# Optimization experiments

Hardware: AMD Instinct MI355X
Metric: run time of the kernel (lower is better)

The kernel has to match this reference:

```python
import jax, jax.numpy as jnp
import numpy as np

N = 100000      # nodes
E = 1600000     # edges
IN = 256        # in_channels
H = 128         # hidden_channels
OUT = 64        # output_channels
B = 64          # graphs in batch
EPS = 1e-5      # BatchNorm eps


def setup_inputs() -> dict:
    key = jax.random.key(0)
    ks = jax.random.split(key, 32)

    def lin_w(k, fan_in, fan_out):
        return (jax.random.normal(k, (fan_in, fan_out), jnp.float32) / np.sqrt(fan_in)).astype(jnp.float32)

    inp = {
        'x': jax.random.normal(ks[0], (N, IN), jnp.float32),
        'edge_index': jax.random.randint(ks[1], (2, E), 0, N, dtype=jnp.int32),
        'batch': jnp.sort(jax.random.randint(ks[2], (N,), 0, B, dtype=jnp.int32)),
        # GCN conv weights (layer 0: IN->H, layers 1,2: H->H)
        'W0': lin_w(ks[3], IN, H), 'b0': jnp.zeros((H,), jnp.float32),
        'W1': lin_w(ks[4], H, H),  'b1': jnp.zeros((H,), jnp.float32),
        'W2': lin_w(ks[5], H, H),  'b2': jnp.zeros((H,), jnp.float32),
        # BatchNorm affine params per layer
        'g0': 1.0 + 0.1 * jax.random.normal(ks[6], (H,), jnp.float32),
        'be0': 0.1 * jax.random.normal(ks[7], (H,), jnp.float32),
        'g1': 1.0 + 0.1 * jax.random.normal(ks[8], (H,), jnp.float32),
        'be1': 0.1 * jax.random.normal(ks[9], (H,), jnp.float32),
        'g2': 1.0 + 0.1 * jax.random.normal(ks[10], (H,), jnp.float32),
        'be2': 0.1 * jax.random.normal(ks[11], (H,), jnp.float32),
        # residual projection (in_channels != hidden_channels)
        'Wres': lin_w(ks[12], IN, H), 'bres': jnp.zeros((H,), jnp.float32),
        # head MLP: Linear(H,H) -> ReLU -> Dropout(eval) -> Linear(H,OUT)
        'Wl0': lin_w(ks[13], H, H), 'bl0': jnp.zeros((H,), jnp.float32),
        'Wl1': lin_w(ks[14], H, OUT), 'bl1': jnp.zeros((OUT,), jnp.float32),
    }
    return inp


def _gcn_layer(h, src, dst, dinv, W, b):
    # PyG GCNConv: linear first, then sym-normalized aggregation with self loops
    h = h @ W                                   # [N, d_out]
    enorm = dinv[src] * dinv[dst]               # [E]
    msg = h[src] * enorm[:, None]               # gather + scale  [E, d_out]
    agg = jax.ops.segment_sum(msg, dst, num_segments=N)
    agg = agg + h * (dinv * dinv)[:, None]      # self-loop contribution (norm = 1/deg)
    return agg + b


def _bn_eval(h, g, be):
    # inference BatchNorm with running_mean=0, running_var=1
    return h * (g / np.sqrt(1.0 + EPS)) + be


def reference(x, edge_index, batch,
              W0, b0, W1, b1, W2, b2,
              g0, be0, g1, be1, g2, be2,
              Wres, bres, Wl0, bl0, Wl1, bl1):
    src, dst = edge_index[0], edge_index[1]
    # degrees with self loops (edge weight 1)
    deg = jax.ops.segment_sum(jnp.ones((E,), jnp.float32), dst, num_segments=N) + 1.0
    dinv = jax.lax.rsqrt(deg)                   # [N]

    Ws, bs, gs, bes = [W0, W1, W2], [b0, b1, b2], [g0, g1, g2], [be0, be1, be2]
    h = x
    for i in range(3):
        h = _gcn_layer(h, src, dst, dinv, Ws[i], bs[i])
        h = jax.nn.relu(_bn_eval(h, gs[i], bes[i]))  # dropout is identity in eval
        if i == 0:
            h = h + (x @ Wres + bres)           # residual projection of original input

    # head MLP on node features
    out = jax.nn.relu(h @ Wl0 + bl0) @ Wl1 + bl1    # [N, OUT]

    # global mean pool over graphs
    counts = jax.ops.segment_sum(jnp.ones((N,), jnp.float32), batch, num_segments=B)
    pooled = jax.ops.segment_sum(h, batch, num_segments=B) / jnp.maximum(counts, 1.0)[:, None]
    return out, pooled
```

## Files before the change

kernel.cpp:

```cpp
#include <hip/hip_runtime.h>
#include <hip/hip_fp16.h>

typedef __half f16;
typedef _Float16 half8 __attribute__((ext_vector_type(8)));
typedef float floatx4 __attribute__((ext_vector_type(4)));

#define NN   100000
#define NE   1600000
#define CIN  256
#define CH   128
#define COUT 64
#define NB   64

#define NBUK 128
#define NPB  782
#define BCAP 32
#define CAPB 20480
#define G1   512
#define EPB  3125
#define CSZ  15104

__global__ void k_sentinel(float* __restrict__ out, int n, float val) {
    int i = blockIdx.x * 256 + threadIdx.x;
    if (i < n) out[i] = val;
}

__global__ void k_init(float* __restrict__ pool, float* __restrict__ cnt,
                       int* __restrict__ gcur) {
    int i = blockIdx.x * 256 + threadIdx.x;
    if (i < NB * CH) pool[i] = 0.0f;
    if (i < NB) cnt[i] = 0.0f;
    if (i < NBUK) gcur[i] = i * CAPB;
}

__global__ __launch_bounds__(256) void k_bin(const int* __restrict__ src,
                                             const int* __restrict__ dst,
                                             int* __restrict__ gcur,
                                             int* __restrict__ stage) {
    __shared__ int bins[NBUK][BCAP];
    __shared__ int bcnt[NBUK];
    __shared__ int fcnt[NBUK];
    __shared__ int fbase[NBUK];
    const int tid = threadIdx.x;
    if (tid < NBUK) bcnt[tid] = 0;
    __syncthreads();
    const int e0 = blockIdx.x * EPB;
    const int e1 = (e0 + EPB < NE) ? e0 + EPB : NE;
    for (int base = e0; base < e1; base += 256) {
        int e = base + tid;
        if (e < e1) {
            int s = src[e], d = dst[e];
            int bk = d / NPB;
            int pk = ((d - bk * NPB) << 17) | s;
            int pos = atomicAdd(&bcnt[bk], 1);
            if (pos < BCAP) {
                bins[bk][pos] = pk;
            } else {
                int gp = atomicAdd(&gcur[bk], 1);
                if (gp < (bk + 1) * CAPB) stage[gp] = pk;
            }
        }
        __syncthreads();
        if (tid < NBUK) {
            int stored = bcnt[tid]; if (stored > BCAP) stored = BCAP;
            int nf = stored & ~15;
            fcnt[tid] = nf;
            if (nf) fbase[tid] = atomicAdd(&gcur[tid], nf);
        }
        __syncthreads();
#pragma unroll
        for (int pass = 0; pass < NBUK / 16; ++pass) {
            int b = pass * 16 + (tid >> 4);
            int sl = tid & 15;
            int nf = fcnt[b];
            int fb = fbase[b];
            for (int k = sl; k < nf; k += 16)
                if (fb + k < (b + 1) * CAPB) stage[fb + k] = bins[b][k];
        }
        __syncthreads();
        if (tid < NBUK) {
            int stored = bcnt[tid]; if (stored > BCAP) stored = BCAP;
            int nf = fcnt[tid];
            for (int k = nf; k < stored; ++k) bins[tid][k - nf] = bins[tid][k];
            bcnt[tid] = stored - nf;
        }
        __syncthreads();
    }
    if (tid < NBUK) {
        int stored = bcnt[tid];
        fcnt[tid] = stored;
        if (stored) fbase[tid] = atomicAdd(&gcur[tid], stored);
    }
    __syncthreads();
#pragma unroll
    for (int pass = 0; pass < NBUK / 16; ++pass) {
        int b = pass * 16 + (tid >> 4);
        int sl = tid & 15;
        int nf = fcnt[b];
        int fb = fbase[b];
        for (int k = sl; k < nf; k += 16)
            if (fb + k < (b + 1) * CAPB) stage[fb + k] = bins[b][k];
    }
}

__global__ void k_gtot(const int* __restrict__ gcur, int* __restrict__ barr,
                       int* __restrict__ rowptr) {
    int lane = threadIdx.x;
    int carry = 0;
    for (int c0 = 0; c0 < NBUK; c0 += 64) {
        int idx = c0 + lane;
        int orig = gcur[idx] - idx * CAPB;
        int v = orig;
#pragma unroll
        for (int off = 1; off < 64; off <<= 1) {
            int t = __shfl_up(v, off);
            if (lane >= off) v += t;
        }
        barr[idx] = v - orig + carry;
        carry += __shfl(v, 63);
    }
    if (lane == 0) rowptr[NN] = NE;
}

__global__ __launch_bounds__(256) void k_csr(const int* __restrict__ gcur,
                                             const int* __restrict__ barr,
                                             const int* __restrict__ stage,
                                             int* __restrict__ rowptr,
                                             int* __restrict__ csr,
                                             float* __restrict__ dinv) {
    __shared__ int hist[NPB];
    __shared__ int lcsr[CSZ];
    const int b = blockIdx.x, tid = threadIdx.x;
    const int nbase = b * NPB;
    const int nloc = (NPB < NN - nbase) ? NPB : NN - nbase;
    const int count = gcur[b] - b * CAPB;
    const int gbase = barr[b];
    const int sb = b * CAPB;
    for (int i = tid; i < NPB; i += 256) hist[i] = 0;
    __syncthreads();
    for (int i = tid; i < count; i += 256)
        atomicAdd(&hist[stage[sb + i] >> 17], 1);
    __syncthreads();
    for (int dl = tid; dl < nloc; dl += 256)
        dinv[nbase + dl] = rsqrtf((float)hist[dl] + 1.0f);
    __syncthreads();
    if (tid < 64) {
        int carry = 0;
        for (int c0 = 0; c0 < NPB; c0 += 64) {
            int idx = c0 + tid;
            int orig = (idx < NPB) ? hist[idx] : 0;
            int v = orig;
#pragma unroll
            for (int off = 1; off < 64; off <<= 1) {
                int t = __shfl_up(v, off);
                if (tid >= off) v += t;
            }
            if (idx < NPB) hist[idx] = v - orig + carry;
            carry += __shfl(v, 63);
        }
    }
    __syncthreads();
    for (int dl = tid; dl < nloc; dl += 256)
        rowptr[nbase + dl] = gbase + hist[dl];
    __syncthreads();
    const bool fits = (count <= CSZ);
    for (int i = tid; i < count; i += 256) {
        int pk = stage[sb + i];
        int dl = pk >> 17, s = pk & 0x1FFFF;
        int pos = atomicAdd(&hist[dl], 1);
        if (fits) lcsr[pos] = s;
        else csr[gbase + pos] = s;
    }
    __syncthreads();
    if (fits)
        for (int i = tid; i < count; i += 256) csr[gbase + i] = lcsr[i];
}

__global__ __launch_bounds__(256) void k_wconv(
        const float* __restrict__ W0, const float* __restrict__ Wres,
        const float* __restrict__ W1, const float* __restrict__ W2,
        const float* __restrict__ Wl0, const float* __restrict__ Wl1,
        half8* __restrict__ F0, half8* __restrict__ Fres,
        half8* __restrict__ F1, half8* __restrict__ F2,
        half8* __restrict__ Fl0, half8* __restrict__ Fl1) {
    int f = blockIdx.x * 256 + threadIdx.x;
    const float* W; half8* F; int M, base;
    if      (f <  4096) { W = W0;   F = F0;   M = 128; base = 0; }
    else if (f <  8192) { W = Wres; F = Fres; M = 128; base = 4096; }
    else if (f < 10240) { W = W1;   F = F1;   M = 128; base = 8192; }
    else if (f < 12288) { W = W2;   F = F2;   M = 128; base = 10240; }
    else if (f < 14336) { W = Wl0;  F = Fl0;  M = 128; base = 12288; }
    else if (f < 15360) { W = Wl1;  F = Fl1;  M = 64;  base = 14336; }
    else return;
    int fl = f - base;
    int lane = fl & 63, fm = lane & 15, g = lane >> 4;
    int rest = fl >> 6;
    int nt = M / 16;
    int t = rest % nt, kt = rest / nt;
    half8 v;
#pragma unroll
    for (int j = 0; j < 8; ++j)
        v[j] = (_Float16)W[(size_t)(kt * 32 + g * 8 + j) * M + t * 16 + fm];
    F[fl] = v;
}

__global__ __launch_bounds__(256) void k_mfma0(const float* __restrict__ x,
                                               const half8* __restrict__ WF,
                                               const half8* __restrict__ WFb,
                                               const float* __restrict__ bres,
                                               const float* __restrict__ dinv,
                                               f16* __restrict__ lout,
                                               f16* __restrict__ rout) {
    constexpr int LP = 72;
    __shared__ __align__(16) _Float16 Al[2][64 * LP];
    const int tid = threadIdx.x;
    const int wave = tid >> 6, lane = tid & 63;
    const int fm = lane & 15, g = lane >> 4;
    const int rb = blockIdx.x * 64;

    const int arow = tid >> 2;
    const int koff = (tid & 3) * 16;
    const int grow = rb + arow;
    const bool live = (grow < NN);
    const float* xp = x + (size_t)(live ? grow : 0) * CIN + koff;

    floatx4 acc[16];
#pragma unroll
    for (int t = 0; t < 16; ++t)
#pragma unroll
        for (int r = 0; r < 4; ++r) acc[t][r] = 0.0f;

    auto ldchunk = [&](int kbase, half8& h0, half8& h1) {
        if (live) {
            float4 a = *(const float4*)(xp + kbase);
            float4 b = *(const float4*)(xp + kbase + 4);
            float4 c = *(const float4*)(xp + kbase + 8);
            float4 d = *(const float4*)(xp + kbase + 12);
            h0[0] = (_Float16)a.x; h0[1] = (_Float16)a.y;
            h0[2] = (_Float16)a.z; h0[3] = (_Float16)a.w;
            h0[4] = (_Float16)b.x; h0[5] = (_Float16)b.y;
            h0[6] = (_Float16)b.z; h0[7] = (_Float16)b.w;
            h1[0] = (_Float16)c.x; h1[1] = (_Float16)c.y;
            h1[2] = (_Float16)c.z; h1[3] = (_Float16)c.w;
            h1[4] = (_Float16)d.x; h1[5] = (_Float16)d.y;
            h1[6] = (_Float16)d.z; h1[7] = (_Float16)d.w;
        } else {
#pragma unroll
            for (int i = 0; i < 8; ++i) { h0[i] = (_Float16)0.0f; h1[i] = (_Float16)0.0f; }
        }
    };

    {
        half8 h0, h1;
        ldchunk(0, h0, h1);
        *(half8*)&Al[0][arow * LP + koff] = h0;
        *(half8*)&Al[0][arow * LP + koff + 8] = h1;
    }
    __syncthreads();

    for (int kt = 0; kt < 4; ++kt) {
        const int cur = kt & 1;
        half8 n0, n1;
        if (kt < 3) ldchunk((kt + 1) * 64, n0, n1);
#pragma unroll
        for (int s = 0; s < 2; ++s) {
            half8 afrag = *(const half8*)&Al[cur][(wave * 16 + fm) * LP + s * 32 + g * 8];
            const int kk = kt * 2 + s;
#pragma unroll
            for (int t = 0; t < 8; ++t)
                acc[t] = __builtin_amdgcn_mfma_f32_16x16x32_f16(
                    afrag, WF[((size_t)kk * 8 + t) * 64 + lane], acc[t], 0, 0, 0);
#pragma unroll
            for (int t = 0; t < 8; ++t)
                acc[8 + t] = __builtin_amdgcn_mfma_f32_16x16x32_f16(
                    afrag, WFb[((size_t)kk * 8 + t) * 64 + lane], acc[8 + t], 0, 0, 0);
        }
        if (kt < 3) {
            *(half8*)&Al[cur ^ 1][arow * LP + koff] = n0;
            *(half8*)&Al[cur ^ 1][arow * LP + koff + 8] = n1;
        }
        __syncthreads();
    }

    const int rloc = wave * 16 + g * 4;
#pragma unroll
    for (int t = 0; t < 8; ++t) {
        int col = t * 16 + fm;
#pragma unroll
        for (int r = 0; r < 4; ++r) {
            int row = rb + rloc + r;
            if (row < NN) lout[(size_t)row * 128 + col] = (f16)(acc[t][r] * dinv[row]);
        }
    }
#pragma unroll
    for (int t = 0; t < 8; ++t) {
        int col = t * 16 + fm;
        float bb = bres[col];
#pragma unroll
        for (int r = 0; r < 4; ++r) {
            int row = rb + rloc + r;
            if (row < NN) rout[(size_t)row * 128 + col] = (f16)(acc[8 + t][r] + bb);
        }
    }
}

__global__ __launch_bounds__(256) void k_lin(const f16* __restrict__ A,
                                             const half8* __restrict__ WF,
                                             const float* __restrict__ dinv,
                                             f16* __restrict__ lout) {
    const int tid = threadIdx.x;
    const int wave = tid >> 6, lane = tid & 63;
    const int fm = lane & 15, g = lane >> 4;
    const int tb = blockIdx.x * 64 + wave * 16;
    const int arow = tb + fm;

    half8 af[4];
#pragma unroll
    for (int kt = 0; kt < 4; ++kt) {
        if (arow < NN) {
            af[kt] = *(const half8*)((const _Float16*)A + (size_t)arow * CH + kt * 32 + g * 8);
        } else {
#pragma unroll
            for (int i = 0; i < 8; ++i) af[kt][i] = (_Float16)0.0f;
        }
    }

    floatx4 acc[8];
#pragma unroll
    for (int t = 0; t < 8; ++t)
#pragma unroll
        for (int r = 0; r < 4; ++r) acc[t][r] = 0.0f;

#pragma unroll
    for (int kt = 0; kt < 4; ++kt)
#pragma unroll
        for (int t = 0; t < 8; ++t)
            acc[t] = __builtin_amdgcn_mfma_f32_16x16x32_f16(
                af[kt], WF[((size_t)kt * 8 + t) * 64 + lane], acc[t], 0, 0, 0);

#pragma unroll
    for (int t = 0; t < 8; ++t) {
        int col = t * 16 + fm;
#pragma unroll
        for (int r = 0; r < 4; ++r) {
            int row = tb + g * 4 + r;
            if (row < NN) lout[(size_t)row * CH + col] = (f16)(acc[t][r] * dinv[row]);
        }
    }
}

__global__ __launch_bounds__(256) void k_head(const f16* __restrict__ A,
                                              const half8* __restrict__ WF0,
                                              const half8* __restrict__ WF1,
                                              const float* __restrict__ bl0,
                                              const float* __restrict__ bl1,
                                              float* __restrict__ outp) {
    constexpr int LP = 136;
    __shared__ __align__(16) _Float16 Hs[64 * LP];
    const int tid = threadIdx.x;
    const int wave = tid >> 6, lane = tid & 63;
    const int fm = lane & 15, g = lane >> 4;
    const int tb = blockIdx.x * 64 + wave * 16;
    const int arow = tb + fm;

    half8 af[4];
#pragma unroll
    for (int kt = 0; kt < 4; ++kt) {
        if (arow < NN) {
            af[kt] = *(const half8*)((const _Float16*)A + (size_t)arow * CH + kt * 32 + g * 8);
        } else {
#pragma unroll
            for (int i = 0; i < 8; ++i) af[kt][i] = (_Float16)0.0f;
        }
    }

    floatx4 acc[8];
#pragma unroll
    for (int t = 0; t < 8; ++t)
#pragma unroll
        for (int r = 0; r < 4; ++r) acc[t][r] = 0.0f;

#pragma unroll
    for (int kt = 0; kt < 4; ++kt)
#pragma unroll
        for (int t = 0; t < 8; ++t)
            acc[t] = __builtin_amdgcn_mfma_f32_16x16x32_f16(
                af[kt], WF0[((size_t)kt * 8 + t) * 64 + lane], acc[t], 0, 0, 0);

    const int lrow = wave * 16 + g * 4;
#pragma unroll
    for (int t = 0; t < 8; ++t) {
        int col = t * 16 + fm;
        float b = bl0[col];
#pragma unroll
        for (int r = 0; r < 4; ++r)
            Hs[(lrow + r) * LP + col] = (_Float16)fmaxf(acc[t][r] + b, 0.0f);
    }
    __syncthreads();

    floatx4 acc2[4];
#pragma unroll
    for (int t = 0; t < 4; ++t)
#pragma unroll
        for (int r = 0; r < 4; ++r) acc2[t][r] = 0.0f;

#pragma unroll
    for (int kt = 0; kt < 4; ++kt) {
        half8 a2 = *(const half8*)&Hs[(wave * 16 + fm) * LP + kt * 32 + g * 8];
#pragma unroll
        for (int t = 0; t < 4; ++t)
            acc2[t] = __builtin_amdgcn_mfma_f32_16x16x32_f16(
                a2, WF1[((size_t)kt * 4 + t) * 64 + lane], acc2[t], 0, 0, 0);
    }

#pragma unroll
    for (int t = 0; t < 4; ++t) {
        int col = t * 16 + fm;
        float b = bl1[col];
#pragma unroll
        for (int r = 0; r < 4; ++r) {
            int row = tb + g * 4 + r;
            if (row < NN) outp[(size_t)row * COUT + col] = acc2[t][r] + b;
        }
    }
}

template <bool RES>
__global__ __launch_bounds__(256) void k_gather(const int* __restrict__ rowptr,
                                                const int* __restrict__ csr,
                                                const float* __restrict__ dinv,
                                                const f16* __restrict__ lin,
                                                const f16* __restrict__ res,
                                                f16* __restrict__ h,
                                                const float* __restrict__ b,
                                                const float* __restrict__ g,
                                                const float* __restrict__ be) {
    const int gw = (blockIdx.x * 256 + threadIdx.x) >> 6;
    const int lane = threadIdx.x & 63;
    if (gw >= NN) return;
    const __half2* lp = (const __half2*)lin;
    const int start = __builtin_amdgcn_readfirstlane(rowptr[gw]);
    const int end   = __builtin_amdgcn_readfirstlane(rowptr[gw + 1]);

    float2 acc = __half22float2(lp[(size_t)gw * 64 + lane]);
    int j = start;
    for (; j + 7 < end; j += 8) {
        int s0 = csr[j],     s1 = csr[j + 1], s2 = csr[j + 2], s3 = csr[j + 3];
        int s4 = csr[j + 4], s5 = csr[j + 5], s6 = csr[j + 6], s7 = csr[j + 7];
        float2 v0 = __half22float2(lp[(size_t)s0 * 64 + lane]);
        float2 v1 = __half22float2(lp[(size_t)s1 * 64 + lane]);
        float2 v2 = __half22float2(lp[(size_t)s2 * 64 + lane]);
        float2 v3 = __half22float2(lp[(size_t)s3 * 64 + lane]);
        float2 v4 = __half22float2(lp[(size_t)s4 * 64 + lane]);
        float2 v5 = __half22float2(lp[(size_t)s5 * 64 + lane]);
        float2 v6 = __half22float2(lp[(size_t)s6 * 64 + lane]);
        float2 v7 = __half22float2(lp[(size_t)s7 * 64 + lane]);
        acc.x += ((v0.x + v1.x) + (v2.x + v3.x)) + ((v4.x + v5.x) + (v6.x + v7.x));
        acc.y += ((v0.y + v1.y) + (v2.y + v3.y)) + ((v4.y + v5.y) + (v6.y + v7.y));
    }
    for (; j + 3 < end; j += 4) {
        int s0 = csr[j], s1 = csr[j + 1], s2 = csr[j + 2], s3 = csr[j + 3];
        float2 v0 = __half22float2(lp[(size_t)s0 * 64 + lane]);
        float2 v1 = __half22float2(lp[(size_t)s1 * 64 + lane]);
        float2 v2 = __half22float2(lp[(size_t)s2 * 64 + lane]);
        float2 v3 = __half22float2(lp[(size_t)s3 * 64 + lane]);
        acc.x += (v0.x + v1.x) + (v2.x + v3.x);
        acc.y += (v0.y + v1.y) + (v2.y + v3.y);
    }
    for (; j < end; ++j) {
        int s = csr[j];
        float2 v = __half22float2(lp[(size_t)s * 64 + lane]);
        acc.x += v.x;
        acc.y += v.y;
    }
    const float inv_sqrt = 0.99999500003749968f;
    float dv = dinv[gw];
    int f = lane * 2;
    float2 bb = *(const float2*)&b[f];
    float2 gg = *(const float2*)&g[f];
    float2 ee = *(const float2*)&be[f];
    float t0 = fmaxf((acc.x * dv + bb.x) * (gg.x * inv_sqrt) + ee.x, 0.0f);
    float t1 = fmaxf((acc.y * dv + bb.y) * (gg.y * inv_sqrt) + ee.y, 0.0f);
    if (RES) {
        float2 rv = __half22float2(((const __half2*)res)[(size_t)gw * 64 + lane]);
        t0 += rv.x;
        t1 += rv.y;
    }
    ((__half2*)h)[(size_t)gw * 64 + lane] = __floats2half2_rn(t0, t1);
}

__global__ void k_count(const int* __restrict__ batch, float* __restrict__ cnt) {
    __shared__ float hist[NB];
    int tid = threadIdx.x;
    if (tid < NB) hist[tid] = 0.0f;
    __syncthreads();
    int n = blockIdx.x * 256 + tid;
    if (n < NN) atomicAdd(&hist[batch[n]], 1.0f);
    __syncthreads();
    if (tid < NB && hist[tid] != 0.0f) atomicAdd(&cnt[tid], hist[tid]);
}

__global__ void k_pool(const f16* __restrict__ h, const int* __restrict__ batch,
                       float* __restrict__ pool) {
    int n0 = blockIdx.x * 64;
    int j = threadIdx.x;
    int cur = batch[n0];
    float acc = 0.0f;
    int nend = (n0 + 64 < NN) ? n0 + 64 : NN;
    for (int n = n0; n < nend; ++n) {
        int b = batch[n];
        if (b != cur) {
            atomicAdd(&pool[cur * CH + j], acc);
            acc = 0.0f;
            cur = b;
        }
        acc += (float)h[(size_t)n * CH + j];
    }
    atomicAdd(&pool[cur * CH + j], acc);
}

__global__ void k_pool_fin(const float* __restrict__ pool,
                           const float* __restrict__ cnt,
                           float* __restrict__ out) {
    int i = blockIdx.x * 256 + threadIdx.x;
    if (i < NB * CH) {
        float c = fmaxf(cnt[i / CH], 1.0f);
        out[i] = pool[i] / c;
    }
}

extern "C" void kernel_launch(void* const* d_in, const int* in_sizes, int n_in,
                              void* d_out, int out_size, void* d_ws, size_t ws_size,
                              hipStream_t stream) {
    float* outp  = (float*)d_out;
    float* poolp = outp + (size_t)NN * COUT;

    const size_t HB = (size_t)NN * CH * 2;
    const size_t LB = (size_t)NN * CH * 2;
    const size_t RB = (size_t)NN * CH * 2;
    const size_t DV = (size_t)NN * 4;
    const size_t RP = 400016;
    const size_t CS = (size_t)NE * 4;
    const size_t GC = 512;
    const size_t BA = 528;
    const size_t PL = (size_t)NB * CH * 4;
    const size_t CT = 256;
    const size_t F0B = 4096 * 16, F1B = 2048 * 16, FLB = 1024 * 16;
    const size_t need = HB + LB + RB + DV + RP + CS + GC + BA + PL + CT
                        + 2 * F0B + 3 * F1B + FLB;
    if (ws_size < need) {
        k_sentinel<<<(out_size + 255) / 256, 256, 0, stream>>>(outp, out_size, 2000.0f);
        return;
    }
    char* p = (char*)d_ws;
    f16*   hbuf   = (f16*)p;               p += HB;
    f16*   lbuf   = (f16*)p;               p += LB;
    f16*   rbuf   = (f16*)p;
    int*   stage  = (int*)p;               p += RB;
    float* dinv   = (float*)p;             p += DV;
    int*   rowptr = (int*)p;               p += RP;
    int*   csr    = (int*)p;               p += CS;
    int*   gcur   = (int*)p;               p += GC;
    int*   barr   = (int*)p;               p += BA;
    float* pool   = (float*)p;             p += PL;
    float* cnt    = (float*)p;             p += CT;
    half8* F0     = (half8*)p;             p += F0B;
    half8* Fres   = (half8*)p;             p += F0B;
    half8* F1     = (half8*)p;             p += F1B;
    half8* F2     = (half8*)p;             p += F1B;
    half8* Fl0    = (half8*)p;             p += F1B;
    half8* Fl1    = (half8*)p;

    const float* x   = (const float*)d_in[0];
    const int*   ei  = (const int*)d_in[1];
    const int*   bat = (const int*)d_in[2];
    const float* W0 = (const float*)d_in[3],  *b0 = (const float*)d_in[4];
    const float* W1 = (const float*)d_in[5],  *b1 = (const float*)d_in[6];
    const float* W2 = (const float*)d_in[7],  *b2 = (const float*)d_in[8];
    const float* g0 = (const float*)d_in[9],  *be0 = (const float*)d_in[10];
    const float* g1 = (const float*)d_in[11], *be1 = (const float*)d_in[12];
    const float* g2 = (const float*)d_in[13], *be2 = (const float*)d_in[14];
    const float* Wres = (const float*)d_in[15], *bres = (const float*)d_in[16];
    const float* Wl0 = (const float*)d_in[17], *bl0 = (const float*)d_in[18];
    const float* Wl1 = (const float*)d_in[19], *bl1 = (const float*)d_in[20];

    const int* src = ei;
    const int* dst = ei + NE;

    const int gRow = (NN + 63) / 64;
    const int gGat = (NN * 64) / 256;

    k_init<<<33, 256, 0, stream>>>(pool, cnt, gcur);
    k_wconv<<<60, 256, 0, stream>>>(W0, Wres, W1, W2, Wl0, Wl1,
                                    F0, Fres, F1, F2, Fl0, Fl1);
    k_bin<<<G1, 256, 0, stream>>>(src, dst, gcur, stage);
    k_gtot<<<1, 64, 0, stream>>>(gcur, barr, rowptr);
    k_csr<<<NBUK, 256, 0, stream>>>(gcur, barr, stage, rowptr, csr, dinv);

    k_mfma0<<<gRow, 256, 0, stream>>>(x, F0, Fres, bres, dinv, lbuf, rbuf);
    k_gather<true><<<gGat, 256, 0, stream>>>(rowptr, csr, dinv, lbuf, rbuf, hbuf, b0, g0, be0);

    k_lin<<<gRow, 256, 0, stream>>>(hbuf, F1, dinv, lbuf);
    k_gather<false><<<gGat, 256, 0, stream>>>(rowptr, csr, dinv, lbuf, nullptr, hbuf, b1, g1, be1);

    k_lin<<<gRow, 256, 0, stream>>>(hbuf, F2, dinv, lbuf);
    k_gather<false><<<gGat, 256, 0, stream>>>(rowptr, csr, dinv, lbuf, nullptr, hbuf, b2, g2, be2);

    k_count<<<(NN + 255) / 256, 256, 0, stream>>>(bat, cnt);
    k_pool<<<gRow, 128, 0, stream>>>(hbuf, bat, pool);
    k_pool_fin<<<(NB * CH + 255) / 256, 256, 0, stream>>>(pool, cnt, poolp);

    k_head<<<gRow, 256, 0, stream>>>(hbuf, Fl0, Fl1, bl0, bl1, outp);
}
```

Before: 694.1 us.

## Stage weight fragments in shared memory for layer-0 MFMA GEMM

Changes the first-layer GEMM (x@W0 and x@Wres) so each wave loads a quarter of the B fragments from global into registers and stores them to a double-buffered LDS tile, instead of every wave reading all B fragments from global directly. The K tile is halved from 64 to 32 and the loop runs 8 iterations, which shrinks the A tile and its padding. The intent is to cut redundant global and L2 traffic for weights and to overlap weight loads with MFMA work. In exchange it adds more LDS traffic and twice as many barriers.

```diff
diff --git a/kernel.cpp b/kernel.cpp
--- a/kernel.cpp
+++ b/kernel.cpp
@@ -211,74 +211,81 @@
                                                const float* __restrict__ dinv,
                                                f16* __restrict__ lout,
                                                f16* __restrict__ rout) {
-    constexpr int LP = 72;
-    __shared__ __align__(16) _Float16 Al[2][64 * LP];
+    constexpr int APAD = 40;
+    __shared__ __align__(16) _Float16 Al[2][64 * APAD];
+    __shared__ __align__(16) _Float16 Bl[2][16 * 512];
     const int tid = threadIdx.x;
     const int wave = tid >> 6, lane = tid & 63;
     const int fm = lane & 15, g = lane >> 4;
     const int rb = blockIdx.x * 64;
 
     const int arow = tid >> 2;
-    const int koff = (tid & 3) * 16;
+    const int koff = (tid & 3) * 8;
     const int grow = rb + arow;
     const bool live = (grow < NN);
     const float* xp = x + (size_t)(live ? grow : 0) * CIN + koff;
 
+    const int bt = wave * 4;
+
     floatx4 acc[16];
 #pragma unroll
     for (int t = 0; t < 16; ++t)
 #pragma unroll
         for (int r = 0; r < 4; ++r) acc[t][r] = 0.0f;
 
-    auto ldchunk = [&](int kbase, half8& h0, half8& h1) {
+    float4 a0, a1;
+    half8 rB[4];
+
+    auto ldA = [&](int kt) {
         if (live) {
-            float4 a = *(const float4*)(xp + kbase);
-            float4 b = *(const float4*)(xp + kbase + 4);
-            float4 c = *(const float4*)(xp + kbase + 8);
-            float4 d = *(const float4*)(xp + kbase + 12);
-            h0[0] = (_Float16)a.x; h0[1] = (_Float16)a.y;
-            h0[2] = (_Float16)a.z; h0[3] = (_Float16)a.w;
-            h0[4] = (_Float16)b.x; h0[5] = (_Float16)b.y;
-            h0[6] = (_Float16)b.z; h0[7] = (_Float16)b.w;
-            h1[0] = (_Float16)c.x; h1[1] = (_Float16)c.y;
-            h1[2] = (_Float16)c.z; h1[3] = (_Float16)c.w;
-            h1[4] = (_Float16)d.x; h1[5] = (_Float16)d.y;
-            h1[6] = (_Float16)d.z; h1[7] = (_Float16)d.w;
+            a0 = *(const float4*)(xp + kt * 32);
+            a1 = *(const float4*)(xp + kt * 32 + 4);
         } else {
-#pragma unroll
-            for (int i = 0; i < 8; ++i) { h0[i] = (_Float16)0.0f; h1[i] = (_Float16)0.0f; }
+            a0 = make_float4(0.f, 0.f, 0.f, 0.f);
+            a1 = make_float4(0.f, 0.f, 0.f, 0.f);
         }
     };
-
-    {
-        half8 h0, h1;
-        ldchunk(0, h0, h1);
-        *(half8*)&Al[0][arow * LP + koff] = h0;
-        *(half8*)&Al[0][arow * LP + koff + 8] = h1;
-    }
-    __syncthreads();
-
-    for (int kt = 0; kt < 4; ++kt) {
+    auto ldB = [&](int kt) {
+#pragma unroll
+        for (int i = 0; i < 4; ++i) {
+            int t = bt + i;
+            rB[i] = (t < 8) ? WF[((size_t)kt * 8 + t) * 64 + lane]
+                            : WFb[((size_t)kt * 8 + (t - 8)) * 64 + lane];
+        }
+    };
+    auto stA = [&](int buf) {
+        half8 h;
+        h[0] = (_Float16)a0.x; h[1] = (_Float16)a0.y;
+        h[2] = (_Float16)a0.z; h[3] = (_Float16)a0.w;
+        h[4] = (_Float16)a1.x; h[5] = (_Float16)a1.y;
+        h[6] = (_Float16)a1.z; h[7] = (_Float16)a1.w;
+        *(half8*)&Al[buf][arow * APAD + koff] = h;
+    };
+    auto stB = [&](int buf) {
+#pragma unroll
+        for (int i = 0; i < 4; ++i)
+            *(half8*)&Bl[buf][(bt + i) * 512 + lane * 8] = rB[i];
+    };
+
+    ldA(0); ldB(0);
+    stA(0); stB(0);
+    __syncthreads();
+
+    for (int kt = 0; kt < 8; ++kt) {
         const int cur = kt & 1;
-        half8 n0, n1;
-        if (kt < 3) ldchunk((kt + 1) * 64, n0, n1);
-#pragma unroll
-        for (int s = 0; s < 2; ++s) {
-            half8 afrag = *(const half8*)&Al[cur][(wave * 16 + fm) * LP + s * 32 + g * 8];
-            const int kk = kt * 2 + s;
-#pragma unroll
-            for (int t = 0; t < 8; ++t)
-                acc[t] = __builtin_amdgcn_mfma_f32_16x16x32_f16(
-                    afrag, WF[((size_t)kk * 8 + t) * 64 + lane], acc[t], 0, 0, 0);
-#pragma unroll
-            for (int t = 0; t < 8; ++t)
-                acc[8 + t] = __builtin_amdgcn_mfma_f32_16x16x32_f16(
-                    afrag, WFb[((size_t)kk * 8 + t) * 64 + lane], acc[8 + t], 0, 0, 0);
-        }
-        if (kt < 3) {
-            *(half8*)&Al[cur ^ 1][arow * LP + koff] = n0;
-            *(half8*)&Al[cur ^ 1][arow * LP + koff + 8] = n1;
-        }
+        if (kt < 7) { ldA(kt + 1); ldB(kt + 1); }
+        half8 afrag = *(const half8*)&Al[cur][(wave * 16 + fm) * APAD + g * 8];
+#pragma unroll
+        for (int t = 0; t < 8; ++t) {
+            half8 bfrag = *(const half8*)&Bl[cur][t * 512 + lane * 8];
+            acc[t] = __builtin_amdgcn_mfma_f32_16x16x32_f16(afrag, bfrag, acc[t], 0, 0, 0);
+        }
+#pragma unroll
+        for (int t = 0; t < 8; ++t) {
+            half8 bfrag = *(const half8*)&Bl[cur][(8 + t) * 512 + lane * 8];
+            acc[8 + t] = __builtin_amdgcn_mfma_f32_16x16x32_f16(afrag, bfrag, acc[8 + t], 0, 0, 0);
+        }
+        if (kt < 7) { stA(cur ^ 1); stB(cur ^ 1); }
         __syncthreads();
     }
 
```

Result: faster. 640.1 us (-7.8%).
